# Kernel tuning notes

Hardware: AMD Instinct MI355X
Metric: run time of the kernel (lower is better)

Reference implementation:

```python
import jax, jax.numpy as jnp
import numpy as np

N_NODES = 100000
N_EDGES = 1200000
D_IN = 16
D_EDGE = 4
H = 64


def setup_inputs() -> dict:
    key = jax.random.key(0)
    ks = jax.random.split(key, 20)
    s = 0.05
    inp = {
        "src": jax.random.randint(ks[0], (N_EDGES,), 0, N_NODES),
        "dst": jax.random.randint(ks[1], (N_EDGES,), 0, N_NODES),
        "t": jax.random.uniform(ks[2], (N_EDGES,), dtype=jnp.float32),
        "x": jax.random.normal(ks[3], (N_NODES, D_IN), dtype=jnp.float32),
        "edge_attr": jax.random.normal(ks[4], (N_EDGES, D_EDGE), dtype=jnp.float32),
        # x_encoder
        "Wx": jax.random.normal(ks[5], (D_IN, H), dtype=jnp.float32) * s,
        "bx": jnp.zeros((H,), dtype=jnp.float32),
        # TransformerConv (heads=1, concat=False)
        "Wq": jax.random.normal(ks[6], (H, H), dtype=jnp.float32) * s,
        "bq": jnp.zeros((H,), dtype=jnp.float32),
        "Wk": jax.random.normal(ks[7], (H, H), dtype=jnp.float32) * s,
        "bk": jnp.zeros((H,), dtype=jnp.float32),
        "Wv": jax.random.normal(ks[8], (H, H), dtype=jnp.float32) * s,
        "bv": jnp.zeros((H,), dtype=jnp.float32),
        "We": jax.random.normal(ks[9], (D_EDGE, H), dtype=jnp.float32) * s,  # lin_edge, bias=False
        "Ws": jax.random.normal(ks[10], (H, H), dtype=jnp.float32) * s,  # lin_skip (root weight)
        "bs": jnp.zeros((H,), dtype=jnp.float32),
        # MLP head
        "W1": jax.random.normal(ks[11], (H, 8), dtype=jnp.float32) * s,
        "b1": jnp.zeros((8,), dtype=jnp.float32),
        "W2": jax.random.normal(ks[12], (8, 1), dtype=jnp.float32) * s,
        "b2": jnp.zeros((1,), dtype=jnp.float32),
    }
    return inp


def reference(src, dst, t, x, edge_attr, Wx, bx, Wq, bq, Wk, bk, Wv, bv, We, Ws, bs, W1, b1, W2, b2):
    # eval mode: dropouts are identity; TGN memory.update_state is a pure
    # side effect and does not influence the returned output.
    xe = x @ Wx + bx                             # [N, H]

    # TransformerConv, heads=1, concat=False, flow src -> dst
    q = xe @ Wq + bq                             # [N, H]
    k = xe @ Wk + bk                             # [N, H]
    v = xe @ Wv + bv                             # [N, H]
    e = edge_attr @ We                           # [E, H]

    k_e = k[src] + e                             # [E, H]
    v_e = v[src] + e                             # [E, H]
    alpha = jnp.sum(q[dst] * k_e, axis=-1) / jnp.sqrt(jnp.float32(H))  # [E]

    # softmax over incoming edges per destination node
    m = jax.ops.segment_max(alpha, dst, num_segments=N_NODES)
    a = jnp.exp(alpha - m[dst])
    denom = jax.ops.segment_sum(a, dst, num_segments=N_NODES)
    w = a / (denom[dst] + 1e-16)                 # [E]

    agg = jax.ops.segment_sum(v_e * w[:, None], dst, num_segments=N_NODES)  # [N, H]
    h_local = agg + (xe @ Ws + bs)               # root/skip connection

    h = h_local[dst]                             # [E, H]
    h = jax.nn.relu(h @ W1 + b1)                 # [E, 8]
    out = (h @ W2 + b2)[:, 0]                    # [E]
    return out
```

## Files before the change

kernel.cpp:

```cpp
#include <hip/hip_runtime.h>

#define H 64
#define CAP 48

#define OFF_M   0
#define OFF_U   256
#define OFF_W   272
#define OFF_C   288
#define OFF_R   292
#define OFF_R0  356
#define OFF_PV  360
#define OFF_PE  488
#define OFF_PS  520
#define OFF_BH1 648
#define OFF_BH2 656
#define CST_N   664

__device__ __forceinline__ unsigned f2bf(float f) {
    unsigned u = __float_as_uint(f);
    u += 0x7fffu + ((u >> 16) & 1u);
    return u >> 16;
}
__device__ __forceinline__ float bf_lo(unsigned u) { return __uint_as_float(u << 16); }
__device__ __forceinline__ float bf_hi(unsigned u) { return __uint_as_float(u & 0xffff0000u); }

__global__ __launch_bounds__(256) void k_fold(
    const float* __restrict__ Wx, const float* __restrict__ bx,
    const float* __restrict__ Wq, const float* __restrict__ bq,
    const float* __restrict__ Wk, const float* __restrict__ bk,
    const float* __restrict__ Wv, const float* __restrict__ bv,
    const float* __restrict__ Ws, const float* __restrict__ bs,
    const float* __restrict__ We, const float* __restrict__ W1,
    const float* __restrict__ b1, float* __restrict__ cst)
{
    __shared__ float sWf[4][16][64];
    __shared__ float sbf[4][64];
    const int t = threadIdx.x;
    const int c = t & 63, m = t >> 6;
    const float* W; const float* b;
    switch (m) {
        case 0:  W = Wq; b = bq; break;
        case 1:  W = Wk; b = bk; break;
        case 2:  W = Wv; b = bv; break;
        default: W = Ws; b = bs; break;
    }
    float acc[16];
#pragma unroll
    for (int i = 0; i < 16; ++i) acc[i] = 0.f;
    float bacc = b[c];
    for (int j = 0; j < 64; ++j) {
        const float wv = W[j * 64 + c];
        bacc += bx[j] * wv;
#pragma unroll
        for (int i = 0; i < 16; ++i) acc[i] += Wx[i * 64 + j] * wv;
    }
#pragma unroll
    for (int i = 0; i < 16; ++i) sWf[m][i][c] = acc[i];
    sbf[m][c] = bacc;
    __syncthreads();

    {
        const int i = t >> 4, j = t & 15;
        float s = 0.f;
        for (int cc = 0; cc < 64; ++cc) s += sWf[0][i][cc] * sWf[1][j][cc];
        cst[OFF_M + i * 16 + j] = s;
    }
    if (t < 16) {
        float su = 0.f, sw = 0.f;
        for (int cc = 0; cc < 64; ++cc) {
            su += sWf[1][t][cc] * sbf[0][cc];
            sw += sWf[0][t][cc] * sbf[1][cc];
        }
        cst[OFF_U + t] = su;
        cst[OFF_W + t] = sw;
    }
    if (t == 0) {
        float s = 0.f;
        for (int cc = 0; cc < 64; ++cc) s += sbf[0][cc] * sbf[1][cc];
        cst[OFF_C] = s;
    }
    if (t < 64) {
        const int j = t >> 4, i = t & 15;
        float s = 0.f;
        for (int cc = 0; cc < 64; ++cc) s += We[j * 64 + cc] * sWf[0][i][cc];
        cst[OFF_R + j * 16 + i] = s;
    }
    if (t < 4) {
        float s = 0.f;
        for (int cc = 0; cc < 64; ++cc) s += We[t * 64 + cc] * sbf[0][cc];
        cst[OFF_R0 + t] = s;
    }
    if (t < 128) {
        const int i = t >> 3, j = t & 7;
        float sv = 0.f, ss = 0.f;
        for (int cc = 0; cc < 64; ++cc) {
            const float w1 = W1[cc * 8 + j];
            sv += sWf[2][i][cc] * w1;
            ss += sWf[3][i][cc] * w1;
        }
        cst[OFF_PV + i * 8 + j] = sv;
        cst[OFF_PS + i * 8 + j] = ss;
    }
    if (t < 32) {
        const int mm = t >> 3, j = t & 7;
        float s = 0.f;
        for (int cc = 0; cc < 64; ++cc) s += We[mm * 64 + cc] * W1[cc * 8 + j];
        cst[OFF_PE + mm * 8 + j] = s;
    }
    if (t < 8) {
        float s1 = 0.f, s2 = 0.f;
        for (int cc = 0; cc < 64; ++cc) {
            const float w1 = W1[cc * 8 + t];
            s1 += sbf[2][cc] * w1;
            s2 += sbf[3][cc] * w1;
        }
        cst[OFF_BH1 + t] = s1;
        cst[OFF_BH2 + t] = s2 + b1[t];
    }
}

__global__ __launch_bounds__(256) void k_fill(
    const int* __restrict__ src, const int* __restrict__ dst,
    const float4* __restrict__ ea4,
    int* __restrict__ cursor, int4* __restrict__ csr, int E)
{
    const int e = blockIdx.x * 256 + threadIdx.x;
    if (e >= E) return;
    const int s = src[e];
    const int d = dst[e];
    const float4 A = ea4[e];
    const int pos = atomicAdd(&cursor[d], 1);
    if (pos < CAP) {
        int4 ent;
        ent.x = s;
        ent.y = e;
        ent.z = (int)(f2bf(A.x) | (f2bf(A.y) << 16));
        ent.w = (int)(f2bf(A.z) | (f2bf(A.w) << 16));
        csr[(size_t)d * CAP + pos] = ent;
    }
}

__global__ __launch_bounds__(256) void k_node_agg(
    const int* __restrict__ degp, const int4* __restrict__ csr,
    const float* __restrict__ x, const float* __restrict__ cst,
    const float* __restrict__ W2, const float* __restrict__ b2,
    float* __restrict__ out, int N)
{
    const int t = threadIdx.x;
    const int l = t & 63;
    const int w = t >> 6;
    const int n = blockIdx.x * 4 + w;
    if (n >= N) return;
    const int grp = l >> 4;
    const int cg  = l & 15;

    const int deg = min(degp[n], CAP);
    const size_t nbase = (size_t)n * CAP;

    const float xd = x[(size_t)n * 16 + cg];

    float y = cst[OFF_U + cg];
#pragma unroll
    for (int i = 0; i < 16; ++i)
        y += __shfl(xd, i) * cst[OFF_M + i * 16 + cg];

    float pr0 = cst[OFF_R + 0 * 16 + cg] * xd;
    float pr1 = cst[OFF_R + 1 * 16 + cg] * xd;
    float pr2 = cst[OFF_R + 2 * 16 + cg] * xd;
    float pr3 = cst[OFF_R + 3 * 16 + cg] * xd;
    float pcd = cst[OFF_W + cg] * xd;
#pragma unroll
    for (int d = 1; d < 16; d <<= 1) {
        pr0 += __shfl_xor(pr0, d);
        pr1 += __shfl_xor(pr1, d);
        pr2 += __shfl_xor(pr2, d);
        pr3 += __shfl_xor(pr3, d);
        pcd += __shfl_xor(pcd, d);
    }
    const float r0 = pr0 + cst[OFF_R0 + 0];
    const float r1 = pr1 + cst[OFF_R0 + 1];
    const float r2 = pr2 + cst[OFF_R0 + 2];
    const float r3 = pr3 + cst[OFF_R0 + 3];
    const float cd = pcd + cst[OFF_C];

    float T = 0.f, S0 = 0.f, S1 = 0.f, S2 = 0.f, S3 = 0.f, den = 0.f;

    for (int base = 0; base < deg; base += 8) {
        const int ia = base + grp;
        const int ib = base + 4 + grp;
        const bool va = ia < deg;
        const bool vb = ib < deg;
        const int4 Ea = csr[nbase + (va ? ia : 0)];
        const int4 Eb = csr[nbase + (vb ? ib : 0)];
        const float xsa = x[(size_t)Ea.x * 16 + cg];
        const float xsb = x[(size_t)Eb.x * 16 + cg];
        {
            const float A0 = bf_lo((unsigned)Ea.z), A1 = bf_hi((unsigned)Ea.z);
            const float A2 = bf_lo((unsigned)Ea.w), A3 = bf_hi((unsigned)Ea.w);
            float p = y * xsa;
            p += __shfl_xor(p, 1);
            p += __shfl_xor(p, 2);
            p += __shfl_xor(p, 4);
            p += __shfl_xor(p, 8);
            p += cd + A0 * r0 + A1 * r1 + A2 * r2 + A3 * r3;
            const float a = va ? __expf(p * 0.125f) : 0.f;
            T += a * xsa;
            S0 += a * A0; S1 += a * A1; S2 += a * A2; S3 += a * A3;
            den += a;
        }
        {
            const float A0 = bf_lo((unsigned)Eb.z), A1 = bf_hi((unsigned)Eb.z);
            const float A2 = bf_lo((unsigned)Eb.w), A3 = bf_hi((unsigned)Eb.w);
            float p = y * xsb;
            p += __shfl_xor(p, 1);
            p += __shfl_xor(p, 2);
            p += __shfl_xor(p, 4);
            p += __shfl_xor(p, 8);
            p += cd + A0 * r0 + A1 * r1 + A2 * r2 + A3 * r3;
            const float a = vb ? __expf(p * 0.125f) : 0.f;
            T += a * xsb;
            S0 += a * A0; S1 += a * A1; S2 += a * A2; S3 += a * A3;
            den += a;
        }
    }

    T   += __shfl_xor(T, 16);   T   += __shfl_xor(T, 32);
    den += __shfl_xor(den, 16); den += __shfl_xor(den, 32);
    S0  += __shfl_xor(S0, 16);  S0  += __shfl_xor(S0, 32);
    S1  += __shfl_xor(S1, 16);  S1  += __shfl_xor(S1, 32);
    S2  += __shfl_xor(S2, 16);  S2  += __shfl_xor(S2, 32);
    S3  += __shfl_xor(S3, 16);  S3  += __shfl_xor(S3, 32);

    const float inv = 1.f / (den + 1e-16f);
    const float Ti = T * inv;

    float hp[8];
#pragma unroll
    for (int j = 0; j < 8; ++j)
        hp[j] = Ti * cst[OFF_PV + cg * 8 + j] + xd * cst[OFF_PS + cg * 8 + j];
#pragma unroll
    for (int j = 0; j < 8; ++j) {
        hp[j] += __shfl_xor(hp[j], 1);
        hp[j] += __shfl_xor(hp[j], 2);
        hp[j] += __shfl_xor(hp[j], 4);
        hp[j] += __shfl_xor(hp[j], 8);
    }
    const float dinv = den * inv;
    float val = b2[0];
#pragma unroll
    for (int j = 0; j < 8; ++j) {
        const float hid = hp[j]
            + inv * (S0 * cst[OFF_PE + 0 * 8 + j] + S1 * cst[OFF_PE + 1 * 8 + j]
                   + S2 * cst[OFF_PE + 2 * 8 + j] + S3 * cst[OFF_PE + 3 * 8 + j])
            + dinv * cst[OFF_BH1 + j] + cst[OFF_BH2 + j];
        val += fmaxf(hid, 0.f) * W2[j];
    }

    for (int i = l; i < deg; i += 64)
        out[csr[nbase + i].y] = val;
}

extern "C" void kernel_launch(void* const* d_in, const int* in_sizes, int n_in,
                              void* d_out, int out_size, void* d_ws, size_t ws_size,
                              hipStream_t stream)
{
    const int*   src = (const int*)d_in[0];
    const int*   dst = (const int*)d_in[1];
    const float* x   = (const float*)d_in[3];
    const float* ea  = (const float*)d_in[4];
    const float* Wx  = (const float*)d_in[5];
    const float* bx  = (const float*)d_in[6];
    const float* Wq  = (const float*)d_in[7];
    const float* bq  = (const float*)d_in[8];
    const float* Wk  = (const float*)d_in[9];
    const float* bk  = (const float*)d_in[10];
    const float* Wv  = (const float*)d_in[11];
    const float* bv  = (const float*)d_in[12];
    const float* We  = (const float*)d_in[13];
    const float* Ws  = (const float*)d_in[14];
    const float* bs  = (const float*)d_in[15];
    const float* W1  = (const float*)d_in[16];
    const float* b1  = (const float*)d_in[17];
    const float* W2  = (const float*)d_in[18];
    const float* b2  = (const float*)d_in[19];

    const int E = in_sizes[0];
    const int N = in_sizes[3] / 16;
    float* out = (float*)d_out;

    int4* csr   = (int4*)d_ws;
    int* cursor = (int*)(csr + (size_t)N * CAP);
    float* cst  = (float*)(cursor + N);

    hipMemsetAsync(cursor, 0, (size_t)N * sizeof(int), stream);

    k_fold<<<1, 256, 0, stream>>>(Wx, bx, Wq, bq, Wk, bk, Wv, bv, Ws, bs,
                                  We, W1, b1, cst);

    k_fill<<<(E + 255) / 256, 256, 0, stream>>>(
        src, dst, (const float4*)ea, cursor, csr, E);

    k_node_agg<<<(N + 3) / 4, 256, 0, stream>>>(
        cursor, csr, x, cst, W2, b2, out, N);
}
```

Before: 299.5 us.

## Fuse memset, fold, fill and aggregation into one cooperative persistent kernel

Replaces the memset plus three kernel launches with a single cooperative kernel that zeroes cursors, runs the weight fold on block 0 while other blocks fill the CSR, and then aggregates nodes in a grid-stride loop, with grid-wide barriers between the phases. This removes launch gaps and idle tails between phases. It adds two grid.sync barriers and caps the grid at 2048 persistent blocks, which may reduce latency hiding compared with the original one-wave-per-node launch. The fallback path also merges the fold into the fill kernel.

```diff
diff --git a/kernel.cpp b/kernel.cpp
--- a/kernel.cpp
+++ b/kernel.cpp
@@ -1,7 +1,12 @@
 #include <hip/hip_runtime.h>
+#include <hip/hip_cooperative_groups.h>
+
+namespace cg = cooperative_groups;
 
 #define H 64
 #define CAP 48
+
+typedef int nint4 __attribute__((ext_vector_type(4)));
 
 #define OFF_M   0
 #define OFF_U   256
@@ -24,14 +29,19 @@
 __device__ __forceinline__ float bf_lo(unsigned u) { return __uint_as_float(u << 16); }
 __device__ __forceinline__ float bf_hi(unsigned u) { return __uint_as_float(u & 0xffff0000u); }
 
-__global__ __launch_bounds__(256) void k_fold(
-    const float* __restrict__ Wx, const float* __restrict__ bx,
-    const float* __restrict__ Wq, const float* __restrict__ bq,
-    const float* __restrict__ Wk, const float* __restrict__ bk,
-    const float* __restrict__ Wv, const float* __restrict__ bv,
-    const float* __restrict__ Ws, const float* __restrict__ bs,
-    const float* __restrict__ We, const float* __restrict__ W1,
-    const float* __restrict__ b1, float* __restrict__ cst)
+struct Params {
+    const int* src; const int* dst; const float4* ea4; const float* x;
+    const float* Wx; const float* bx;
+    const float* Wq; const float* bq;
+    const float* Wk; const float* bk;
+    const float* Wv; const float* bv;
+    const float* We; const float* Ws; const float* bs;
+    const float* W1; const float* b1; const float* W2; const float* b2;
+    int* cursor; nint4* csr; float* cst; float* out;
+    int N, E;
+};
+
+__device__ void do_fold(const Params& P, float* __restrict__ cst)
 {
     __shared__ float sWf[4][16][64];
     __shared__ float sbf[4][64];
@@ -39,10 +49,10 @@
     const int c = t & 63, m = t >> 6;
     const float* W; const float* b;
     switch (m) {
-        case 0:  W = Wq; b = bq; break;
-        case 1:  W = Wk; b = bk; break;
-        case 2:  W = Wv; b = bv; break;
-        default: W = Ws; b = bs; break;
+        case 0:  W = P.Wq; b = P.bq; break;
+        case 1:  W = P.Wk; b = P.bk; break;
+        case 2:  W = P.Wv; b = P.bv; break;
+        default: W = P.Ws; b = P.bs; break;
     }
     float acc[16];
 #pragma unroll
@@ -50,9 +60,9 @@
     float bacc = b[c];
     for (int j = 0; j < 64; ++j) {
         const float wv = W[j * 64 + c];
-        bacc += bx[j] * wv;
-#pragma unroll
-        for (int i = 0; i < 16; ++i) acc[i] += Wx[i * 64 + j] * wv;
+        bacc += P.bx[j] * wv;
+#pragma unroll
+        for (int i = 0; i < 16; ++i) acc[i] += P.Wx[i * 64 + j] * wv;
     }
 #pragma unroll
     for (int i = 0; i < 16; ++i) sWf[m][i][c] = acc[i];
@@ -82,19 +92,19 @@
     if (t < 64) {
         const int j = t >> 4, i = t & 15;
         float s = 0.f;
-        for (int cc = 0; cc < 64; ++cc) s += We[j * 64 + cc] * sWf[0][i][cc];
+        for (int cc = 0; cc < 64; ++cc) s += P.We[j * 64 + cc] * sWf[0][i][cc];
         cst[OFF_R + j * 16 + i] = s;
     }
     if (t < 4) {
         float s = 0.f;
-        for (int cc = 0; cc < 64; ++cc) s += We[t * 64 + cc] * sbf[0][cc];
+        for (int cc = 0; cc < 64; ++cc) s += P.We[t * 64 + cc] * sbf[0][cc];
         cst[OFF_R0 + t] = s;
     }
     if (t < 128) {
         const int i = t >> 3, j = t & 7;
         float sv = 0.f, ss = 0.f;
         for (int cc = 0; cc < 64; ++cc) {
-            const float w1 = W1[cc * 8 + j];
+            const float w1 = P.W1[cc * 8 + j];
             sv += sWf[2][i][cc] * w1;
             ss += sWf[3][i][cc] * w1;
         }
@@ -104,202 +114,242 @@
     if (t < 32) {
         const int mm = t >> 3, j = t & 7;
         float s = 0.f;
-        for (int cc = 0; cc < 64; ++cc) s += We[mm * 64 + cc] * W1[cc * 8 + j];
+        for (int cc = 0; cc < 64; ++cc) s += P.We[mm * 64 + cc] * P.W1[cc * 8 + j];
         cst[OFF_PE + mm * 8 + j] = s;
     }
     if (t < 8) {
         float s1 = 0.f, s2 = 0.f;
         for (int cc = 0; cc < 64; ++cc) {
-            const float w1 = W1[cc * 8 + t];
+            const float w1 = P.W1[cc * 8 + t];
             s1 += sbf[2][cc] * w1;
             s2 += sbf[3][cc] * w1;
         }
         cst[OFF_BH1 + t] = s1;
-        cst[OFF_BH2 + t] = s2 + b1[t];
-    }
-}
-
-__global__ __launch_bounds__(256) void k_fill(
-    const int* __restrict__ src, const int* __restrict__ dst,
-    const float4* __restrict__ ea4,
-    int* __restrict__ cursor, int4* __restrict__ csr, int E)
-{
-    const int e = blockIdx.x * 256 + threadIdx.x;
-    if (e >= E) return;
-    const int s = src[e];
-    const int d = dst[e];
-    const float4 A = ea4[e];
-    const int pos = atomicAdd(&cursor[d], 1);
+        cst[OFF_BH2 + t] = s2 + P.b1[t];
+    }
+}
+
+__device__ __forceinline__ void fill_edge(const Params& P, int e)
+{
+    const int s = P.src[e];
+    const int d = P.dst[e];
+    const float4 A = P.ea4[e];
+    const int pos = atomicAdd(&P.cursor[d], 1);
     if (pos < CAP) {
-        int4 ent;
+        nint4 ent;
         ent.x = s;
         ent.y = e;
         ent.z = (int)(f2bf(A.x) | (f2bf(A.y) << 16));
         ent.w = (int)(f2bf(A.z) | (f2bf(A.w) << 16));
-        csr[(size_t)d * CAP + pos] = ent;
-    }
-}
-
-__global__ __launch_bounds__(256) void k_node_agg(
-    const int* __restrict__ degp, const int4* __restrict__ csr,
-    const float* __restrict__ x, const float* __restrict__ cst,
-    const float* __restrict__ W2, const float* __restrict__ b2,
-    float* __restrict__ out, int N)
+        P.csr[(size_t)d * CAP + pos] = ent;
+    }
+}
+
+__device__ __forceinline__ void agg_nodes(
+    const Params& P, const float* __restrict__ cst, int gw, int stride, int l)
+{
+    const int grp = l >> 4;
+    const int cg_ = l & 15;
+
+    for (int n = gw; n < P.N; n += stride) {
+        const int deg = min(P.cursor[n], CAP);
+        const size_t nbase = (size_t)n * CAP;
+
+        const float xd = P.x[(size_t)n * 16 + cg_];
+
+        float y = cst[OFF_U + cg_];
+#pragma unroll
+        for (int i = 0; i < 16; ++i)
+            y += __shfl(xd, i) * cst[OFF_M + i * 16 + cg_];
+
+        float pr0 = cst[OFF_R + 0 * 16 + cg_] * xd;
+        float pr1 = cst[OFF_R + 1 * 16 + cg_] * xd;
+        float pr2 = cst[OFF_R + 2 * 16 + cg_] * xd;
+        float pr3 = cst[OFF_R + 3 * 16 + cg_] * xd;
+        float pcd = cst[OFF_W + cg_] * xd;
+#pragma unroll
+        for (int d = 1; d < 16; d <<= 1) {
+            pr0 += __shfl_xor(pr0, d);
+            pr1 += __shfl_xor(pr1, d);
+            pr2 += __shfl_xor(pr2, d);
+            pr3 += __shfl_xor(pr3, d);
+            pcd += __shfl_xor(pcd, d);
+        }
+        const float r0 = pr0 + cst[OFF_R0 + 0];
+        const float r1 = pr1 + cst[OFF_R0 + 1];
+        const float r2 = pr2 + cst[OFF_R0 + 2];
+        const float r3 = pr3 + cst[OFF_R0 + 3];
+        const float cd = pcd + cst[OFF_C];
+
+        float T = 0.f, S0 = 0.f, S1 = 0.f, S2 = 0.f, S3 = 0.f, den = 0.f;
+
+        for (int base = 0; base < deg; base += 8) {
+            const int ia = base + grp;
+            const int ib = base + 4 + grp;
+            const bool va = ia < deg;
+            const bool vb = ib < deg;
+            const nint4 Ea = P.csr[nbase + (va ? ia : 0)];
+            const nint4 Eb = P.csr[nbase + (vb ? ib : 0)];
+            const float xsa = P.x[(size_t)Ea.x * 16 + cg_];
+            const float xsb = P.x[(size_t)Eb.x * 16 + cg_];
+            {
+                const float A0 = bf_lo((unsigned)Ea.z), A1 = bf_hi((unsigned)Ea.z);
+                const float A2 = bf_lo((unsigned)Ea.w), A3 = bf_hi((unsigned)Ea.w);
+                float p = y * xsa;
+                p += __shfl_xor(p, 1);
+                p += __shfl_xor(p, 2);
+                p += __shfl_xor(p, 4);
+                p += __shfl_xor(p, 8);
+                p += cd + A0 * r0 + A1 * r1 + A2 * r2 + A3 * r3;
+                const float a = va ? __expf(p * 0.125f) : 0.f;
+                T += a * xsa;
+                S0 += a * A0; S1 += a * A1; S2 += a * A2; S3 += a * A3;
+                den += a;
+            }
+            {
+                const float A0 = bf_lo((unsigned)Eb.z), A1 = bf_hi((unsigned)Eb.z);
+                const float A2 = bf_lo((unsigned)Eb.w), A3 = bf_hi((unsigned)Eb.w);
+                float p = y * xsb;
+                p += __shfl_xor(p, 1);
+                p += __shfl_xor(p, 2);
+                p += __shfl_xor(p, 4);
+                p += __shfl_xor(p, 8);
+                p += cd + A0 * r0 + A1 * r1 + A2 * r2 + A3 * r3;
+                const float a = vb ? __expf(p * 0.125f) : 0.f;
+                T += a * xsb;
+                S0 += a * A0; S1 += a * A1; S2 += a * A2; S3 += a * A3;
+                den += a;
+            }
+        }
+
+        T   += __shfl_xor(T, 16);   T   += __shfl_xor(T, 32);
+        den += __shfl_xor(den, 16); den += __shfl_xor(den, 32);
+        S0  += __shfl_xor(S0, 16);  S0  += __shfl_xor(S0, 32);
+        S1  += __shfl_xor(S1, 16);  S1  += __shfl_xor(S1, 32);
+        S2  += __shfl_xor(S2, 16);  S2  += __shfl_xor(S2, 32);
+        S3  += __shfl_xor(S3, 16);  S3  += __shfl_xor(S3, 32);
+
+        const float inv = 1.f / (den + 1e-16f);
+        const float Ti = T * inv;
+
+        float hp[8];
+#pragma unroll
+        for (int j = 0; j < 8; ++j)
+            hp[j] = Ti * cst[OFF_PV + cg_ * 8 + j] + xd * cst[OFF_PS + cg_ * 8 + j];
+#pragma unroll
+        for (int j = 0; j < 8; ++j) {
+            hp[j] += __shfl_xor(hp[j], 1);
+            hp[j] += __shfl_xor(hp[j], 2);
+            hp[j] += __shfl_xor(hp[j], 4);
+            hp[j] += __shfl_xor(hp[j], 8);
+        }
+        const float dinv = den * inv;
+        float val = P.b2[0];
+#pragma unroll
+        for (int j = 0; j < 8; ++j) {
+            const float hid = hp[j]
+                + inv * (S0 * cst[OFF_PE + 0 * 8 + j] + S1 * cst[OFF_PE + 1 * 8 + j]
+                       + S2 * cst[OFF_PE + 2 * 8 + j] + S3 * cst[OFF_PE + 3 * 8 + j])
+                + dinv * cst[OFF_BH1 + j] + cst[OFF_BH2 + j];
+            val += fmaxf(hid, 0.f) * P.W2[j];
+        }
+
+        for (int i = l; i < deg; i += 64)
+            P.out[P.csr[nbase + i].y] = val;
+    }
+}
+
+__global__ __launch_bounds__(256) void k_mega(Params P)
 {
     const int t = threadIdx.x;
-    const int l = t & 63;
-    const int w = t >> 6;
-    const int n = blockIdx.x * 4 + w;
-    if (n >= N) return;
-    const int grp = l >> 4;
-    const int cg  = l & 15;
-
-    const int deg = min(degp[n], CAP);
-    const size_t nbase = (size_t)n * CAP;
-
-    const float xd = x[(size_t)n * 16 + cg];
-
-    float y = cst[OFF_U + cg];
-#pragma unroll
-    for (int i = 0; i < 16; ++i)
-        y += __shfl(xd, i) * cst[OFF_M + i * 16 + cg];
-
-    float pr0 = cst[OFF_R + 0 * 16 + cg] * xd;
-    float pr1 = cst[OFF_R + 1 * 16 + cg] * xd;
-    float pr2 = cst[OFF_R + 2 * 16 + cg] * xd;
-    float pr3 = cst[OFF_R + 3 * 16 + cg] * xd;
-    float pcd = cst[OFF_W + cg] * xd;
-#pragma unroll
-    for (int d = 1; d < 16; d <<= 1) {
-        pr0 += __shfl_xor(pr0, d);
-        pr1 += __shfl_xor(pr1, d);
-        pr2 += __shfl_xor(pr2, d);
-        pr3 += __shfl_xor(pr3, d);
-        pcd += __shfl_xor(pcd, d);
-    }
-    const float r0 = pr0 + cst[OFF_R0 + 0];
-    const float r1 = pr1 + cst[OFF_R0 + 1];
-    const float r2 = pr2 + cst[OFF_R0 + 2];
-    const float r3 = pr3 + cst[OFF_R0 + 3];
-    const float cd = pcd + cst[OFF_C];
-
-    float T = 0.f, S0 = 0.f, S1 = 0.f, S2 = 0.f, S3 = 0.f, den = 0.f;
-
-    for (int base = 0; base < deg; base += 8) {
-        const int ia = base + grp;
-        const int ib = base + 4 + grp;
-        const bool va = ia < deg;
-        const bool vb = ib < deg;
-        const int4 Ea = csr[nbase + (va ? ia : 0)];
-        const int4 Eb = csr[nbase + (vb ? ib : 0)];
-        const float xsa = x[(size_t)Ea.x * 16 + cg];
-        const float xsb = x[(size_t)Eb.x * 16 + cg];
-        {
-            const float A0 = bf_lo((unsigned)Ea.z), A1 = bf_hi((unsigned)Ea.z);
-            const float A2 = bf_lo((unsigned)Ea.w), A3 = bf_hi((unsigned)Ea.w);
-            float p = y * xsa;
-            p += __shfl_xor(p, 1);
-            p += __shfl_xor(p, 2);
-            p += __shfl_xor(p, 4);
-            p += __shfl_xor(p, 8);
-            p += cd + A0 * r0 + A1 * r1 + A2 * r2 + A3 * r3;
-            const float a = va ? __expf(p * 0.125f) : 0.f;
-            T += a * xsa;
-            S0 += a * A0; S1 += a * A1; S2 += a * A2; S3 += a * A3;
-            den += a;
-        }
-        {
-            const float A0 = bf_lo((unsigned)Eb.z), A1 = bf_hi((unsigned)Eb.z);
-            const float A2 = bf_lo((unsigned)Eb.w), A3 = bf_hi((unsigned)Eb.w);
-            float p = y * xsb;
-            p += __shfl_xor(p, 1);
-            p += __shfl_xor(p, 2);
-            p += __shfl_xor(p, 4);
-            p += __shfl_xor(p, 8);
-            p += cd + A0 * r0 + A1 * r1 + A2 * r2 + A3 * r3;
-            const float a = vb ? __expf(p * 0.125f) : 0.f;
-            T += a * xsb;
-            S0 += a * A0; S1 += a * A1; S2 += a * A2; S3 += a * A3;
-            den += a;
-        }
-    }
-
-    T   += __shfl_xor(T, 16);   T   += __shfl_xor(T, 32);
-    den += __shfl_xor(den, 16); den += __shfl_xor(den, 32);
-    S0  += __shfl_xor(S0, 16);  S0  += __shfl_xor(S0, 32);
-    S1  += __shfl_xor(S1, 16);  S1  += __shfl_xor(S1, 32);
-    S2  += __shfl_xor(S2, 16);  S2  += __shfl_xor(S2, 32);
-    S3  += __shfl_xor(S3, 16);  S3  += __shfl_xor(S3, 32);
-
-    const float inv = 1.f / (den + 1e-16f);
-    const float Ti = T * inv;
-
-    float hp[8];
-#pragma unroll
-    for (int j = 0; j < 8; ++j)
-        hp[j] = Ti * cst[OFF_PV + cg * 8 + j] + xd * cst[OFF_PS + cg * 8 + j];
-#pragma unroll
-    for (int j = 0; j < 8; ++j) {
-        hp[j] += __shfl_xor(hp[j], 1);
-        hp[j] += __shfl_xor(hp[j], 2);
-        hp[j] += __shfl_xor(hp[j], 4);
-        hp[j] += __shfl_xor(hp[j], 8);
-    }
-    const float dinv = den * inv;
-    float val = b2[0];
-#pragma unroll
-    for (int j = 0; j < 8; ++j) {
-        const float hid = hp[j]
-            + inv * (S0 * cst[OFF_PE + 0 * 8 + j] + S1 * cst[OFF_PE + 1 * 8 + j]
-                   + S2 * cst[OFF_PE + 2 * 8 + j] + S3 * cst[OFF_PE + 3 * 8 + j])
-            + dinv * cst[OFF_BH1 + j] + cst[OFF_BH2 + j];
-        val += fmaxf(hid, 0.f) * W2[j];
-    }
-
-    for (int i = l; i < deg; i += 64)
-        out[csr[nbase + i].y] = val;
+    cg::grid_group grid = cg::this_grid();
+    const int gsz = (int)gridDim.x;
+
+    for (int i = blockIdx.x * 256 + t; i < P.N; i += gsz * 256)
+        P.cursor[i] = 0;
+    grid.sync();
+
+    if (blockIdx.x == 0) {
+        do_fold(P, P.cst);
+    } else {
+        for (int e = (blockIdx.x - 1) * 256 + t; e < P.E; e += (gsz - 1) * 256)
+            fill_edge(P, e);
+    }
+    grid.sync();
+
+    agg_nodes(P, P.cst, blockIdx.x * 4 + (t >> 6), gsz * 4, t & 63);
+}
+
+__global__ __launch_bounds__(256) void k_fill_fb(Params P)
+{
+    if (blockIdx.x == 0) {
+        do_fold(P, P.cst);
+        return;
+    }
+    const int e = (blockIdx.x - 1) * 256 + threadIdx.x;
+    if (e < P.E) fill_edge(P, e);
+}
+
+__global__ __launch_bounds__(256) void k_agg_fb(Params P)
+{
+    const int t = threadIdx.x;
+    const int n = blockIdx.x * 4 + (t >> 6);
+    if (n >= P.N) return;
+    agg_nodes(P, P.cst, n, 0x40000000, t & 63);
 }
 
 extern "C" void kernel_launch(void* const* d_in, const int* in_sizes, int n_in,
                               void* d_out, int out_size, void* d_ws, size_t ws_size,
                               hipStream_t stream)
 {
-    const int*   src = (const int*)d_in[0];
-    const int*   dst = (const int*)d_in[1];
-    const float* x   = (const float*)d_in[3];
-    const float* ea  = (const float*)d_in[4];
-    const float* Wx  = (const float*)d_in[5];
-    const float* bx  = (const float*)d_in[6];
-    const float* Wq  = (const float*)d_in[7];
-    const float* bq  = (const float*)d_in[8];
-    const float* Wk  = (const float*)d_in[9];
-    const float* bk  = (const float*)d_in[10];
-    const float* Wv  = (const float*)d_in[11];
-    const float* bv  = (const float*)d_in[12];
-    const float* We  = (const float*)d_in[13];
-    const float* Ws  = (const float*)d_in[14];
-    const float* bs  = (const float*)d_in[15];
-    const float* W1  = (const float*)d_in[16];
-    const float* b1  = (const float*)d_in[17];
-    const float* W2  = (const float*)d_in[18];
-    const float* b2  = (const float*)d_in[19];
-
-    const int E = in_sizes[0];
-    const int N = in_sizes[3] / 16;
-    float* out = (float*)d_out;
-
-    int4* csr   = (int4*)d_ws;
-    int* cursor = (int*)(csr + (size_t)N * CAP);
-    float* cst  = (float*)(cursor + N);
-
-    hipMemsetAsync(cursor, 0, (size_t)N * sizeof(int), stream);
-
-    k_fold<<<1, 256, 0, stream>>>(Wx, bx, Wq, bq, Wk, bk, Wv, bv, Ws, bs,
-                                  We, W1, b1, cst);
-
-    k_fill<<<(E + 255) / 256, 256, 0, stream>>>(
-        src, dst, (const float4*)ea, cursor, csr, E);
-
-    k_node_agg<<<(N + 3) / 4, 256, 0, stream>>>(
-        cursor, csr, x, cst, W2, b2, out, N);
-}
+    Params P;
+    P.src = (const int*)d_in[0];
+    P.dst = (const int*)d_in[1];
+    P.x   = (const float*)d_in[3];
+    P.ea4 = (const float4*)d_in[4];
+    P.Wx  = (const float*)d_in[5];
+    P.bx  = (const float*)d_in[6];
+    P.Wq  = (const float*)d_in[7];
+    P.bq  = (const float*)d_in[8];
+    P.Wk  = (const float*)d_in[9];
+    P.bk  = (const float*)d_in[10];
+    P.Wv  = (const float*)d_in[11];
+    P.bv  = (const float*)d_in[12];
+    P.We  = (const float*)d_in[13];
+    P.Ws  = (const float*)d_in[14];
+    P.bs  = (const float*)d_in[15];
+    P.W1  = (const float*)d_in[16];
+    P.b1  = (const float*)d_in[17];
+    P.W2  = (const float*)d_in[18];
+    P.b2  = (const float*)d_in[19];
+
+    P.E = in_sizes[0];
+    P.N = in_sizes[3] / 16;
+    P.out = (float*)d_out;
+
+    P.csr    = (nint4*)d_ws;
+    P.cursor = (int*)(P.csr + (size_t)P.N * CAP);
+    P.cst    = (float*)(P.cursor + P.N);
+
+    bool done = false;
+    int blocksPerCU = 0;
+    if (hipOccupancyMaxActiveBlocksPerMultiprocessor(
+            &blocksPerCU, (const void*)k_mega, 256, 0) == hipSuccess &&
+        blocksPerCU > 0) {
+        int grid = blocksPerCU * 256;
+        if (grid > 2048) grid = 2048;
+        if (grid >= 64) {
+            void* args[] = { &P };
+            if (hipLaunchCooperativeKernel((const void*)k_mega, dim3(grid),
+                                           dim3(256), args, 0, stream) == hipSuccess)
+                done = true;
+        }
+    }
+
+    if (!done) {
+        hipMemsetAsync(P.cursor, 0, (size_t)P.N * sizeof(int), stream);
+        const int nbE = (P.E + 255) / 256;
+        k_fill_fb<<<nbE + 1, 256, 0, stream>>>(P);
+        k_agg_fb<<<(P.N + 3) / 4, 256, 0, stream>>>(P);
+    }
+}
```

New measurement: 584.7 us. 1.95x slower.
